# Performance work log

Hardware: AMD Instinct MI355X
Metric: run time of the kernel (lower is better)

Reference implementation:

```python
import jax, jax.numpy as jnp
import numpy as np

RADIUS = 8
EPSILON = 0.01


def _diff_x(x, r):
    left = x[..., r:2 * r + 1, :]
    middle = x[..., 2 * r + 1:, :] - x[..., :-2 * r - 1, :]
    right = x[..., -1:, :] - x[..., -2 * r - 1:-r - 1, :]
    return jnp.concatenate([left, middle, right], axis=-2)


def _diff_y(x, r):
    left = x[..., r:2 * r + 1]
    middle = x[..., 2 * r + 1:] - x[..., :-2 * r - 1]
    right = x[..., -1:] - x[..., -2 * r - 1:-r - 1]
    return jnp.concatenate([left, middle, right], axis=-1)


def box_filter(x, r):
    # x: (N, C, H, W) -> windowed mean over (2r+1)x(2r+1) with reflect padding
    x = jnp.pad(x, ((0, 0), (0, 0), (r, r), (r, r)), mode='reflect')
    x = jnp.cumsum(x, axis=-2)
    x = _diff_x(x, r)
    x = jnp.cumsum(x, axis=-1)
    x = _diff_y(x, r)
    return x[..., r:-r, r:-r] / float((2 * r + 1) ** 2)


def setup_inputs() -> dict:
    key = jax.random.key(0)
    k1, k2 = jax.random.split(key)
    B, C, H, W = 4, 3, 1024, 1024
    I = jax.random.uniform(k1, (B, C, H, W), dtype=jnp.float32)
    p = jax.random.uniform(k2, (B, 1, H, W), dtype=jnp.float32)
    return {"I": I, "p": p}


def reference(I, p) -> jnp.ndarray:
    r, eps = RADIUS, EPSILON
    B, C, H, W = I.shape

    mean_I = box_filter(I, r)                     # (B,C,H,W)
    mean_p = box_filter(p, r)                     # (B,1,H,W)
    mean_Ip = box_filter(I * p, r)                # (B,C,H,W)
    cov_Ip = mean_Ip - mean_I * mean_p            # (B,C,H,W)

    # second moments: (B,C,C,H,W) via reshape to (B*C, C, H, W) for the box filter
    II = I[:, :, None] * I[:, None]               # (B,C,C,H,W)
    mean_II = box_filter(II.reshape(B * C, C, H, W), r).reshape(B, C, C, H, W)
    cov_II = mean_II - mean_I[:, :, None] * mean_I[:, None]

    eye = jnp.eye(C, dtype=I.dtype).reshape(1, C, C, 1, 1)
    S = cov_II + eps * eye                        # (B,C,C,H,W)

    # per-pixel CxC solve: move pixel dims to batch
    S_px = jnp.transpose(S, (0, 3, 4, 1, 2))      # (B,H,W,C,C)
    rhs = jnp.transpose(cov_Ip, (0, 2, 3, 1))[..., None]  # (B,H,W,C,1)
    a = jnp.linalg.solve(S_px, rhs)[..., 0]       # (B,H,W,C)
    a = jnp.transpose(a, (0, 3, 1, 2))            # (B,C,H,W)

    a_mean_I = jnp.einsum('bchw,bchw->bhw', a, mean_I)
    b = mean_p - a_mean_I[:, None]                # (B,1,H,W)

    mean_a = box_filter(a, r)
    mean_b = box_filter(b, r)

    q = jnp.einsum('bchw,bchw->bhw', mean_a, I) + mean_b[:, 0]
    return q[:, None]                             # (B,1,H,W)
```

## Files before the change

### kernel.cpp

```cpp
#include <hip/hip_runtime.h>

#define HH 1024
#define WW 1024
#define NB 4
#define RR 8
#define NCH1 13
#define NCH2 4
#define NXCD 8
#define VSEG1 4
#define NSEG1 (HH / VSEG1)
#define NBLK1 (NB * NSEG1)
#define LDSW1 1040
#define VSEG2 8
#define NSEG2 (HH / VSEG2)
#define TW 512
#define NBLK2 (NB * NSEG2 * 2)
#define LDSW2 544
#define INV_AREA (1.0f/289.0f)
#define EPS_REG 0.01f

typedef float f4 __attribute__((ext_vector_type(4)));
typedef _Float16 h4 __attribute__((ext_vector_type(4)));
typedef float f2 __attribute__((ext_vector_type(2)));
typedef _Float16 h2 __attribute__((ext_vector_type(2)));

__device__ __forceinline__ int refl(int j, int n) {
    int k = j < 0 ? -j : j;
    return k >= n ? 2 * n - 2 - k : k;
}

__device__ __forceinline__ void derived13(f4 i0, f4 i1, f4 i2, f4 pp, f4* d) {
    d[0] = i0; d[1] = i1; d[2] = i2; d[3] = pp;
    d[4] = i0 * pp; d[5] = i1 * pp; d[6] = i2 * pp;
    d[7] = i0 * i0; d[8] = i0 * i1; d[9] = i0 * i2;
    d[10] = i1 * i1; d[11] = i1 * i2; d[12] = i2 * i2;
}


__global__ __launch_bounds__(256, 2) void gf_stage1(
    const float* __restrict__ I, const float* __restrict__ P,
    _Float16* __restrict__ A, _Float16* __restrict__ Bc)
{
    __shared__ float lds[NCH1][LDSW1];
    const int tid = threadIdx.x;
    const int xcd = blockIdx.x & (NXCD - 1);
    const int rank = blockIdx.x >> 3;
    const int bz = xcd >> 1;
    const int seg = (xcd & 1) * 128 + rank;
    const int y0 = seg * VSEG1;
    const int c0 = 4 * tid;
    const float* Ib = I + (size_t)bz * 3 * HH * WW;
    const float* Pb = P + (size_t)bz * HH * WW;

    f4 vs[NCH1];
    #pragma unroll
    for (int ch = 0; ch < NCH1; ++ch) { vs[ch] = (f4){0.f, 0.f, 0.f, 0.f}; }

    for (int dy = -RR; dy <= RR; ++dy) {
        int row = refl(y0 + dy, HH);
        size_t rb = (size_t)row * WW + c0;
        f4 i0 = *(const f4*)(Ib + rb);
        f4 i1 = *(const f4*)(Ib + (size_t)HH * WW + rb);
        f4 i2 = *(const f4*)(Ib + (size_t)2 * HH * WW + rb);
        f4 pp = *(const f4*)(Pb + rb);
        f4 d[NCH1]; derived13(i0, i1, i2, pp, d);
        #pragma unroll
        for (int ch = 0; ch < NCH1; ++ch) vs[ch] += d[ch];
    }

    for (int y = y0; y < y0 + VSEG1; ++y) {
        #pragma unroll
        for (int ch = 0; ch < NCH1; ++ch)
            *(f4*)&lds[ch][8 + c0] = vs[ch];
        if (tid <= 2) {
            #pragma unroll
            for (int j = 0; j < 4; ++j) {
                int c = c0 + j;
                if (c >= 1 && c <= 8) {
                    #pragma unroll
                    for (int ch = 0; ch < NCH1; ++ch) lds[ch][8 - c] = vs[ch][j];
                }
            }
        }
        if (tid >= 253) {
            #pragma unroll
            for (int j = 0; j < 4; ++j) {
                int c = c0 + j;
                if (c >= 1015 && c <= 1022) {
                    #pragma unroll
                    for (int ch = 0; ch < NCH1; ++ch) lds[ch][1032 + (1022 - c)] = vs[ch][j];
                }
            }
        }
        const bool upd = (y + 1 < y0 + VSEG1);
        f4 ai0, ai1, ai2, ap, si0, si1, si2, sp;
        if (upd) {
            int ra = refl(y + 1 + RR, HH);
            int rs = refl(y - RR, HH);
            size_t rba = (size_t)ra * WW + c0;
            size_t rbs = (size_t)rs * WW + c0;
            ai0 = *(const f4*)(Ib + rba);
            ai1 = *(const f4*)(Ib + (size_t)HH * WW + rba);
            ai2 = *(const f4*)(Ib + (size_t)2 * HH * WW + rba);
            ap  = *(const f4*)(Pb + rba);
            si0 = *(const f4*)(Ib + rbs);
            si1 = *(const f4*)(Ib + (size_t)HH * WW + rbs);
            si2 = *(const f4*)(Ib + (size_t)2 * HH * WW + rbs);
            sp  = *(const f4*)(Pb + rbs);
        }
        __syncthreads();

        f4 m[NCH1];
        #pragma unroll
        for (int ch = 0; ch < NCH1; ++ch) {
            float vv[20];
            #pragma unroll
            for (int k = 0; k < 5; ++k)
                ((f4*)vv)[k] = *(const f4*)&lds[ch][c0 + 4 * k];
            float s = (((vv[0]+vv[1])+(vv[2]+vv[3])) + ((vv[4]+vv[5])+(vv[6]+vv[7])))
                    + (((vv[8]+vv[9])+(vv[10]+vv[11])) + ((vv[12]+vv[13])+(vv[14]+vv[15])))
                    + vv[16];
            f4 mm;
            mm[0] = s;
            s += vv[17] - vv[0]; mm[1] = s;
            s += vv[18] - vv[1]; mm[2] = s;
            s += vv[19] - vv[2]; mm[3] = s;
            m[ch] = mm * INV_AREA;
        }

        f4 oa0, oa1, oa2, ob;
        #pragma unroll
        for (int j = 0; j < 4; ++j) {
            float m0 = m[0][j], m1 = m[1][j], m2 = m[2][j], m3 = m[3][j];
            float r0 = m[4][j] - m0 * m3;
            float r1 = m[5][j] - m1 * m3;
            float r2 = m[6][j] - m2 * m3;
            float S00 = m[7][j]  - m0 * m0 + EPS_REG;
            float S01 = m[8][j]  - m0 * m1;
            float S02 = m[9][j]  - m0 * m2;
            float S11 = m[10][j] - m1 * m1 + EPS_REG;
            float S12 = m[11][j] - m1 * m2;
            float S22 = m[12][j] - m2 * m2 + EPS_REG;
            float A0 = S11 * S22 - S12 * S12;
            float B0 = S02 * S12 - S01 * S22;
            float C0 = S01 * S12 - S02 * S11;
            float D0 = S00 * S22 - S02 * S02;
            float E0 = S01 * S02 - S00 * S12;
            float F0 = S00 * S11 - S01 * S01;
            float det = S00 * A0 + S01 * B0 + S02 * C0;
            float inv = 1.0f / det;
            float a0 = (A0 * r0 + B0 * r1 + C0 * r2) * inv;
            float a1 = (B0 * r0 + D0 * r1 + E0 * r2) * inv;
            float a2 = (C0 * r0 + E0 * r1 + F0 * r2) * inv;
            float bb = m3 - (a0 * m0 + a1 * m1 + a2 * m2);
            oa0[j] = a0; oa1[j] = a1; oa2[j] = a2; ob[j] = bb;
        }
        size_t obase = (size_t)y * WW + c0;
        *(h4*)(A + (size_t)(bz * 3 + 0) * HH * WW + obase) = __builtin_convertvector(oa0, h4);
        *(h4*)(A + (size_t)(bz * 3 + 1) * HH * WW + obase) = __builtin_convertvector(oa1, h4);
        *(h4*)(A + (size_t)(bz * 3 + 2) * HH * WW + obase) = __builtin_convertvector(oa2, h4);
        *(h4*)(Bc + (size_t)bz * HH * WW + obase) = __builtin_convertvector(ob, h4);
        __syncthreads();

        if (upd) {
            f4 d[NCH1];
            derived13(ai0, ai1, ai2, ap, d);
            #pragma unroll
            for (int ch = 0; ch < NCH1; ++ch) vs[ch] += d[ch];
            derived13(si0, si1, si2, sp, d);
            #pragma unroll
            for (int ch = 0; ch < NCH1; ++ch) vs[ch] -= d[ch];
        }
    }
}

__device__ __forceinline__ f2 hwin2(const float* ldsrow, int c0) {
    const f2* wp = (const f2*)(ldsrow + c0);
    f2 w0 = wp[0], w1 = wp[1], w2 = wp[2], w3 = wp[3];
    f2 w4 = wp[4], w5 = wp[5], w6 = wp[6], w7 = wp[7], w8 = wp[8];
    f2 e = ((w0 + w1) + (w2 + w3)) + ((w4 + w5) + (w6 + w7));
    float s0 = e[0] + e[1] + w8[0];
    float s1 = s0 - w0[0] + w8[1];
    f2 r; r[0] = s0 * INV_AREA; r[1] = s1 * INV_AREA;
    return r;
}

__global__ __launch_bounds__(256, 2) void gf_stage2(
    const float* __restrict__ I, const _Float16* __restrict__ A,
    const _Float16* __restrict__ Bc, float* __restrict__ Q)
{
    __shared__ float lds[NCH2][LDSW2];
    const int tid = threadIdx.x;
    const int xcd = blockIdx.x & (NXCD - 1);
    const int rank = blockIdx.x >> 3;
    const int bz = xcd >> 1;
    const int seg = (xcd & 1) * 64 + (rank >> 1);
    const int y0 = seg * VSEG2;
    const int wstart = (rank & 1) * TW;
    const int c0 = 2 * tid;
    const int gc = wstart + c0;
    const _Float16* A0p = A + (size_t)(bz * 3 + 0) * HH * WW;
    const _Float16* A1p = A + (size_t)(bz * 3 + 1) * HH * WW;
    const _Float16* A2p = A + (size_t)(bz * 3 + 2) * HH * WW;
    const _Float16* Bp  = Bc + (size_t)bz * HH * WW;
    const float* Ib  = I + (size_t)bz * 3 * HH * WW;

    const bool isHalo = tid < 16;
    const int hraw = (tid < 8) ? (wstart - 8 + tid) : (wstart + TW + (tid - 8));
    const int hg = refl(hraw, WW);
    const int hpos = (tid < 8) ? tid : (8 + TW + (tid - 8));

    f2 vs[NCH2];
    float hs[NCH2];
    #pragma unroll
    for (int ch = 0; ch < NCH2; ++ch) { vs[ch] = (f2){0.f, 0.f}; hs[ch] = 0.f; }

    for (int dy = -RR; dy <= RR; ++dy) {
        int row = refl(y0 + dy, HH);
        size_t rb = (size_t)row * WW;
        vs[0] += __builtin_convertvector(*(const h2*)(A0p + rb + gc), f2);
        vs[1] += __builtin_convertvector(*(const h2*)(A1p + rb + gc), f2);
        vs[2] += __builtin_convertvector(*(const h2*)(A2p + rb + gc), f2);
        vs[3] += __builtin_convertvector(*(const h2*)(Bp + rb + gc), f2);
        if (isHalo) {
            hs[0] += (float)A0p[rb + hg];
            hs[1] += (float)A1p[rb + hg];
            hs[2] += (float)A2p[rb + hg];
            hs[3] += (float)Bp[rb + hg];
        }
    }

    for (int y = y0; y < y0 + VSEG2; ++y) {
        #pragma unroll
        for (int ch = 0; ch < NCH2; ++ch)
            *(f2*)&lds[ch][8 + c0] = vs[ch];
        if (isHalo) {
            #pragma unroll
            for (int ch = 0; ch < NCH2; ++ch) lds[ch][hpos] = hs[ch];
        }
        const bool upd = (y + 1 < y0 + VSEG2);
        f2 aa0, aa1, aa2, ab, sa0, sa1, sa2, sb;
        float ha0, ha1, ha2, hab, hb0, hb1, hb2, hbb;
        size_t rbq = (size_t)y * WW;
        f2 i0 = *(const f2*)(Ib + rbq + gc);
        f2 i1 = *(const f2*)(Ib + (size_t)HH * WW + rbq + gc);
        f2 i2 = *(const f2*)(Ib + (size_t)2 * HH * WW + rbq + gc);
        if (upd) {
            int ra = refl(y + 1 + RR, HH);
            int rs = refl(y - RR, HH);
            size_t rba = (size_t)ra * WW;
            size_t rbs = (size_t)rs * WW;
            aa0 = __builtin_convertvector(*(const h2*)(A0p + rba + gc), f2);
            aa1 = __builtin_convertvector(*(const h2*)(A1p + rba + gc), f2);
            aa2 = __builtin_convertvector(*(const h2*)(A2p + rba + gc), f2);
            ab  = __builtin_convertvector(*(const h2*)(Bp + rba + gc), f2);
            sa0 = __builtin_convertvector(*(const h2*)(A0p + rbs + gc), f2);
            sa1 = __builtin_convertvector(*(const h2*)(A1p + rbs + gc), f2);
            sa2 = __builtin_convertvector(*(const h2*)(A2p + rbs + gc), f2);
            sb  = __builtin_convertvector(*(const h2*)(Bp + rbs + gc), f2);
            if (isHalo) {
                ha0 = (float)A0p[rba + hg]; ha1 = (float)A1p[rba + hg];
                ha2 = (float)A2p[rba + hg]; hab = (float)Bp[rba + hg];
                hb0 = (float)A0p[rbs + hg]; hb1 = (float)A1p[rbs + hg];
                hb2 = (float)A2p[rbs + hg]; hbb = (float)Bp[rbs + hg];
            }
        }
        __syncthreads();

        f2 m[NCH2];
        #pragma unroll
        for (int ch = 0; ch < NCH2; ++ch)
            m[ch] = hwin2(&lds[ch][0], c0);

        f2 qv = m[0] * i0 + m[1] * i1 + m[2] * i2 + m[3];
        *(f2*)(Q + (size_t)bz * HH * WW + rbq + gc) = qv;
        __syncthreads();

        if (upd) {
            vs[0] += aa0 - sa0;
            vs[1] += aa1 - sa1;
            vs[2] += aa2 - sa2;
            vs[3] += ab - sb;
            if (isHalo) {
                hs[0] += ha0 - hb0; hs[1] += ha1 - hb1;
                hs[2] += ha2 - hb2; hs[3] += hab - hbb;
            }
        }
    }
}

extern "C" void kernel_launch(void* const* d_in, const int* in_sizes, int n_in,
                              void* d_out, int out_size, void* d_ws, size_t ws_size,
                              hipStream_t stream) {
    const float* I = (const float*)d_in[0];
    const float* P = (const float*)d_in[1];
    float* Q = (float*)d_out;
    _Float16* A = (_Float16*)d_ws;
    _Float16* Bc = A + (size_t)NB * 3 * HH * WW;
    gf_stage1<<<NBLK1, 256, 0, stream>>>(I, P, A, Bc);
    gf_stage2<<<NBLK2, 256, 0, stream>>>(I, A, Bc, Q);
}
```

Before: 81.89 us.

## Split stage1 rows into half-width tiles with halo threads and remap stage2 blocks

Stage1 now gives each block a 512-column half-row tile with 128 threads, instead of a full 1024-column row with 256 threads. Sixteen halo threads keep their own running sums for the 8 reflected or neighbouring columns on each side. This halves the LDS footprint per block and doubles the block count, aiming for more resident blocks per CU and better latency hiding. The cost is redundant halo loads and arithmetic, plus divergence inside the halo wave. Stage2's block-to-tile mapping also changes so the XCD parity selects the column half rather than the row half, which alters L2 locality across XCDs.

Result: slower. 99.15 us (+21.1%).

```diff
diff --git a/kernel.cpp b/kernel.cpp
--- a/kernel.cpp
+++ b/kernel.cpp
@@ -8,13 +8,12 @@
 #define NCH2 4
 #define NXCD 8
 #define VSEG1 4
-#define NSEG1 (HH / VSEG1)
-#define NBLK1 (NB * NSEG1)
-#define LDSW1 1040
+#define TW1 512
+#define NBLK1 (NB * (HH / VSEG1) * 2)
+#define LDSW1 536
 #define VSEG2 8
-#define NSEG2 (HH / VSEG2)
 #define TW 512
-#define NBLK2 (NB * NSEG2 * 2)
+#define NBLK2 (NB * (HH / VSEG2) * 2)
 #define LDSW2 544
 #define INV_AREA (1.0f/289.0f)
 #define EPS_REG 0.01f
@@ -36,8 +35,15 @@
     d[10] = i1 * i1; d[11] = i1 * i2; d[12] = i2 * i2;
 }
 
-
-__global__ __launch_bounds__(256, 2) void gf_stage1(
+__device__ __forceinline__ void derived13s(float i0, float i1, float i2, float pp, float* d) {
+    d[0] = i0; d[1] = i1; d[2] = i2; d[3] = pp;
+    d[4] = i0 * pp; d[5] = i1 * pp; d[6] = i2 * pp;
+    d[7] = i0 * i0; d[8] = i0 * i1; d[9] = i0 * i2;
+    d[10] = i1 * i1; d[11] = i1 * i2; d[12] = i2 * i2;
+}
+
+
+__global__ __launch_bounds__(128, 2) void gf_stage1(
     const float* __restrict__ I, const float* __restrict__ P,
     _Float16* __restrict__ A, _Float16* __restrict__ Bc)
 {
@@ -46,67 +52,78 @@
     const int xcd = blockIdx.x & (NXCD - 1);
     const int rank = blockIdx.x >> 3;
     const int bz = xcd >> 1;
-    const int seg = (xcd & 1) * 128 + rank;
-    const int y0 = seg * VSEG1;
+    const int wstart = (xcd & 1) * TW1;
+    const int y0 = rank * VSEG1;
     const int c0 = 4 * tid;
+    const int gc = wstart + c0;
     const float* Ib = I + (size_t)bz * 3 * HH * WW;
     const float* Pb = P + (size_t)bz * HH * WW;
 
+    const bool isHalo = tid < 16;
+    const int hraw = (tid < 8) ? (wstart - 8 + tid) : (wstart + TW1 + (tid - 8));
+    const int hg = refl(hraw, WW);
+    const int hpos = (tid < 8) ? tid : (512 + tid);
+
     f4 vs[NCH1];
+    float hs[NCH1];
     #pragma unroll
-    for (int ch = 0; ch < NCH1; ++ch) { vs[ch] = (f4){0.f, 0.f, 0.f, 0.f}; }
+    for (int ch = 0; ch < NCH1; ++ch) { vs[ch] = (f4){0.f, 0.f, 0.f, 0.f}; hs[ch] = 0.f; }
 
     for (int dy = -RR; dy <= RR; ++dy) {
         int row = refl(y0 + dy, HH);
-        size_t rb = (size_t)row * WW + c0;
-        f4 i0 = *(const f4*)(Ib + rb);
-        f4 i1 = *(const f4*)(Ib + (size_t)HH * WW + rb);
-        f4 i2 = *(const f4*)(Ib + (size_t)2 * HH * WW + rb);
-        f4 pp = *(const f4*)(Pb + rb);
+        size_t rb = (size_t)row * WW;
+        f4 i0 = *(const f4*)(Ib + rb + gc);
+        f4 i1 = *(const f4*)(Ib + (size_t)HH * WW + rb + gc);
+        f4 i2 = *(const f4*)(Ib + (size_t)2 * HH * WW + rb + gc);
+        f4 pp = *(const f4*)(Pb + rb + gc);
         f4 d[NCH1]; derived13(i0, i1, i2, pp, d);
         #pragma unroll
         for (int ch = 0; ch < NCH1; ++ch) vs[ch] += d[ch];
+        if (isHalo) {
+            float j0 = Ib[rb + hg];
+            float j1 = Ib[(size_t)HH * WW + rb + hg];
+            float j2 = Ib[(size_t)2 * HH * WW + rb + hg];
+            float jp = Pb[rb + hg];
+            float ds[NCH1]; derived13s(j0, j1, j2, jp, ds);
+            #pragma unroll
+            for (int ch = 0; ch < NCH1; ++ch) hs[ch] += ds[ch];
+        }
     }
 
     for (int y = y0; y < y0 + VSEG1; ++y) {
         #pragma unroll
         for (int ch = 0; ch < NCH1; ++ch)
             *(f4*)&lds[ch][8 + c0] = vs[ch];
-        if (tid <= 2) {
-            #pragma unroll
-            for (int j = 0; j < 4; ++j) {
-                int c = c0 + j;
-                if (c >= 1 && c <= 8) {
-                    #pragma unroll
-                    for (int ch = 0; ch < NCH1; ++ch) lds[ch][8 - c] = vs[ch][j];
-                }
-            }
-        }
-        if (tid >= 253) {
-            #pragma unroll
-            for (int j = 0; j < 4; ++j) {
-                int c = c0 + j;
-                if (c >= 1015 && c <= 1022) {
-                    #pragma unroll
-                    for (int ch = 0; ch < NCH1; ++ch) lds[ch][1032 + (1022 - c)] = vs[ch][j];
-                }
-            }
+        if (isHalo) {
+            #pragma unroll
+            for (int ch = 0; ch < NCH1; ++ch) lds[ch][hpos] = hs[ch];
         }
         const bool upd = (y + 1 < y0 + VSEG1);
         f4 ai0, ai1, ai2, ap, si0, si1, si2, sp;
+        float hai0, hai1, hai2, hap, hsi0, hsi1, hsi2, hsp;
         if (upd) {
             int ra = refl(y + 1 + RR, HH);
             int rs = refl(y - RR, HH);
-            size_t rba = (size_t)ra * WW + c0;
-            size_t rbs = (size_t)rs * WW + c0;
-            ai0 = *(const f4*)(Ib + rba);
-            ai1 = *(const f4*)(Ib + (size_t)HH * WW + rba);
-            ai2 = *(const f4*)(Ib + (size_t)2 * HH * WW + rba);
-            ap  = *(const f4*)(Pb + rba);
-            si0 = *(const f4*)(Ib + rbs);
-            si1 = *(const f4*)(Ib + (size_t)HH * WW + rbs);
-            si2 = *(const f4*)(Ib + (size_t)2 * HH * WW + rbs);
-            sp  = *(const f4*)(Pb + rbs);
+            size_t rba = (size_t)ra * WW;
+            size_t rbs = (size_t)rs * WW;
+            ai0 = *(const f4*)(Ib + rba + gc);
+            ai1 = *(const f4*)(Ib + (size_t)HH * WW + rba + gc);
+            ai2 = *(const f4*)(Ib + (size_t)2 * HH * WW + rba + gc);
+            ap  = *(const f4*)(Pb + rba + gc);
+            si0 = *(const f4*)(Ib + rbs + gc);
+            si1 = *(const f4*)(Ib + (size_t)HH * WW + rbs + gc);
+            si2 = *(const f4*)(Ib + (size_t)2 * HH * WW + rbs + gc);
+            sp  = *(const f4*)(Pb + rbs + gc);
+            if (isHalo) {
+                hai0 = Ib[rba + hg];
+                hai1 = Ib[(size_t)HH * WW + rba + hg];
+                hai2 = Ib[(size_t)2 * HH * WW + rba + hg];
+                hap  = Pb[rba + hg];
+                hsi0 = Ib[rbs + hg];
+                hsi1 = Ib[(size_t)HH * WW + rbs + hg];
+                hsi2 = Ib[(size_t)2 * HH * WW + rbs + hg];
+                hsp  = Pb[rbs + hg];
+            }
         }
         __syncthreads();
 
@@ -155,7 +172,7 @@
             float bb = m3 - (a0 * m0 + a1 * m1 + a2 * m2);
             oa0[j] = a0; oa1[j] = a1; oa2[j] = a2; ob[j] = bb;
         }
-        size_t obase = (size_t)y * WW + c0;
+        size_t obase = (size_t)y * WW + gc;
         *(h4*)(A + (size_t)(bz * 3 + 0) * HH * WW + obase) = __builtin_convertvector(oa0, h4);
         *(h4*)(A + (size_t)(bz * 3 + 1) * HH * WW + obase) = __builtin_convertvector(oa1, h4);
         *(h4*)(A + (size_t)(bz * 3 + 2) * HH * WW + obase) = __builtin_convertvector(oa2, h4);
@@ -170,6 +187,15 @@
             derived13(si0, si1, si2, sp, d);
             #pragma unroll
             for (int ch = 0; ch < NCH1; ++ch) vs[ch] -= d[ch];
+            if (isHalo) {
+                float ds[NCH1];
+                derived13s(hai0, hai1, hai2, hap, ds);
+                #pragma unroll
+                for (int ch = 0; ch < NCH1; ++ch) hs[ch] += ds[ch];
+                derived13s(hsi0, hsi1, hsi2, hsp, ds);
+                #pragma unroll
+                for (int ch = 0; ch < NCH1; ++ch) hs[ch] -= ds[ch];
+            }
         }
     }
 }
@@ -194,9 +220,8 @@
     const int xcd = blockIdx.x & (NXCD - 1);
     const int rank = blockIdx.x >> 3;
     const int bz = xcd >> 1;
-    const int seg = (xcd & 1) * 64 + (rank >> 1);
-    const int y0 = seg * VSEG2;
-    const int wstart = (rank & 1) * TW;
+    const int wstart = (xcd & 1) * TW;
+    const int y0 = rank * VSEG2;
     const int c0 = 2 * tid;
     const int gc = wstart + c0;
     const _Float16* A0p = A + (size_t)(bz * 3 + 0) * HH * WW;
@@ -297,6 +322,6 @@
     float* Q = (float*)d_out;
     _Float16* A = (_Float16*)d_ws;
     _Float16* Bc = A + (size_t)NB * 3 * HH * WW;
-    gf_stage1<<<NBLK1, 256, 0, stream>>>(I, P, A, Bc);
+    gf_stage1<<<NBLK1, 128, 0, stream>>>(I, P, A, Bc);
     gf_stage2<<<NBLK2, 256, 0, stream>>>(I, A, Bc, Q);
 }
```
